# Kernel tuning notes

Measured on AMD Instinct MI355X. Metric: run time of the kernel, lower is better.

Reference implementation:

```python
import jax, jax.numpy as jnp
from jax import lax
import numpy as np

B, C, H, W = 32, 3, 224, 224
NUM_CLASSES = 100
K = 3  # kernel size
OUT1 = 32


def _bn(x, g, b, m, v, eps=1e-5):
    # eval-mode batchnorm over channel dim of NCHW
    inv = g / jnp.sqrt(v + eps)
    return x * inv[None, :, None, None] + (b - m * inv)[None, :, None, None]


def _conv(x, w, pad=1):
    return lax.conv_general_dilated(
        x, w, (1, 1), ((pad, pad), (pad, pad)),
        dimension_numbers=('NCHW', 'OIHW', 'NCHW'))


def _maxpool2(x):
    return lax.reduce_window(x, -jnp.inf, lax.max, (1, 1, 2, 2), (1, 1, 2, 2), 'VALID')


def setup_inputs() -> dict:
    key = jax.random.key(0)
    ks = jax.random.split(key, 32)
    n = lambda k, s, sc=0.05: jax.random.normal(k, s, jnp.float32) * sc
    u = lambda k, s: jax.random.uniform(k, s, jnp.float32, 0.5, 1.5)
    inp = {
        'x': jax.random.normal(ks[0], (B, C, H, W), jnp.float32),
        # weight_gen MLP: Linear(3,128)->ReLU->Linear(128,256)->ReLU->Linear(256, 32*3*3*3)
        'w1': n(ks[1], (128, C)), 'b1': n(ks[2], (128,)),
        'w2': n(ks[3], (256, 128)), 'b2': n(ks[4], (256,)),
        'w3': n(ks[5], (OUT1 * C * K * K, 256)), 'b3': n(ks[6], (OUT1 * C * K * K,)),
        # bias_gen: Linear(3, 32)
        'wb': n(ks[7], (OUT1, C)), 'bb': n(ks[8], (OUT1,)),
        'conv2_w': n(ks[9], (64, 32, 3, 3)), 'conv2_b': n(ks[10], (64,)),
        'conv3_w': n(ks[11], (128, 64, 3, 3)), 'conv3_b': n(ks[12], (128,)),
        'bn1_g': 1.0 + n(ks[13], (32,)), 'bn1_b': n(ks[14], (32,)), 'bn1_m': n(ks[15], (32,)), 'bn1_v': u(ks[16], (32,)),
        'bn2_g': 1.0 + n(ks[17], (64,)), 'bn2_b': n(ks[18], (64,)), 'bn2_m': n(ks[19], (64,)), 'bn2_v': u(ks[20], (64,)),
        'bn3_g': 1.0 + n(ks[21], (128,)), 'bn3_b': n(ks[22], (128,)), 'bn3_m': n(ks[23], (128,)), 'bn3_v': u(ks[24], (128,)),
        'fc_w': n(ks[25], (NUM_CLASSES, 128)), 'fc_b': n(ks[26], (NUM_CLASSES,)),
    }
    return inp


def reference(x, w1, b1, w2, b2, w3, b3, wb, bb, conv2_w, conv2_b, conv3_w, conv3_b,
              bn1_g, bn1_b, bn1_m, bn1_v, bn2_g, bn2_b, bn2_m, bn2_v,
              bn3_g, bn3_b, bn3_m, bn3_v, fc_w, fc_b):
    Bx = x.shape[0]
    # DynamicConv2D: channel indicator is all-ones since C == max_in_channels
    ind = jnp.ones((Bx, C), x.dtype)
    h = jax.nn.relu(ind @ w1.T + b1)
    h = jax.nn.relu(h @ w2.T + b2)
    dyn_w = (h @ w3.T + b3).reshape(Bx, OUT1, C, K, K)  # per-sample [O,I,k,k]
    dyn_b = ind @ wb.T + bb                             # per-sample [O]
    # vmap over batch: one single-image conv per sample with its own weights
    y = jax.vmap(lambda xi, wi, bi: _conv(xi[None], wi)[0] + bi[:, None, None])(x, dyn_w, dyn_b)
    y = jax.nn.relu(_bn(y, bn1_g, bn1_b, bn1_m, bn1_v))
    y = _maxpool2(y)
    y = jax.nn.relu(_bn(_conv(y, conv2_w) + conv2_b[None, :, None, None], bn2_g, bn2_b, bn2_m, bn2_v))
    y = _maxpool2(y)
    y = jax.nn.relu(_bn(_conv(y, conv3_w) + conv3_b[None, :, None, None], bn3_g, bn3_b, bn3_m, bn3_v))
    y = y.mean(axis=(2, 3))  # AdaptiveAvgPool2d((1,1)) + flatten
    # dropout is identity in eval
    return y @ fc_w.T + fc_b
```

## Files before the change

### kernel.cpp

```cpp
#include <hip/hip_runtime.h>
#include <hip/hip_bf16.h>

#define BATCH 32
#define HW1 224

typedef __attribute__((ext_vector_type(8))) short short8;
typedef __attribute__((ext_vector_type(4))) float floatx4;

static __device__ __forceinline__ unsigned short f2bf(float f) {
    unsigned int u = __float_as_uint(f);
    unsigned int r = (u + 0x7fffu + ((u >> 16) & 1u)) >> 16;
    return (unsigned short)r;
}

__global__ __launch_bounds__(256) void gen_dynw_repack(
    const float* __restrict__ w1, const float* __restrict__ b1,
    const float* __restrict__ w2, const float* __restrict__ b2,
    const float* __restrict__ w3, const float* __restrict__ b3,
    const float* __restrict__ conv2_w, const float* __restrict__ conv3_w,
    const float* __restrict__ wb, const float* __restrict__ bb,
    const float* __restrict__ conv2_b, const float* __restrict__ conv3_b,
    const float* __restrict__ bn1_g, const float* __restrict__ bn1_b,
    const float* __restrict__ bn1_m, const float* __restrict__ bn1_v,
    const float* __restrict__ bn2_g, const float* __restrict__ bn2_b,
    const float* __restrict__ bn2_m, const float* __restrict__ bn2_v,
    const float* __restrict__ bn3_g, const float* __restrict__ bn3_b,
    const float* __restrict__ bn3_m, const float* __restrict__ bn3_v,
    float* __restrict__ dwt,
    unsigned short* __restrict__ wrep2, unsigned short* __restrict__ wrep3,
    float* __restrict__ bn1_s, float* __restrict__ bn1_t,
    float* __restrict__ bn2_s, float* __restrict__ bn2_t,
    float* __restrict__ bn3_s, float* __restrict__ bn3_t,
    float* __restrict__ feat)
{
    __shared__ float h1s[128];
    __shared__ float h2s[256];
    const int blk = blockIdx.x;
    const int t = threadIdx.x;
    if (blk < 216) {
        if (t < 128) {
            float s = b1[t] + w1[t*3+0] + w1[t*3+1] + w1[t*3+2];
            h1s[t] = fmaxf(s, 0.f);
        }
        __syncthreads();
        {
            float s = b2[t];
            const float* wr = w2 + (size_t)t*128;
#pragma unroll 4
            for (int k = 0; k < 128; k += 4) {
                float4 wv = *(const float4*)(wr + k);
                s = fmaf(wv.x, h1s[k  ], s);
                s = fmaf(wv.y, h1s[k+1], s);
                s = fmaf(wv.z, h1s[k+2], s);
                s = fmaf(wv.w, h1s[k+3], s);
            }
            h2s[t] = fmaxf(s, 0.f);
        }
        __syncthreads();
        const int wave = t >> 6, lane = t & 63;
        const int row = blk*4 + wave;
        float4 wv = *(const float4*)(w3 + (size_t)row*256 + lane*4);
        float4 hv = *(const float4*)&h2s[lane*4];
        float s = wv.x*hv.x + wv.y*hv.y + wv.z*hv.z + wv.w*hv.w;
#pragma unroll
        for (int m = 1; m < 64; m <<= 1) s += __shfl_xor(s, m);
        if (lane == 0) {
            int oc = row / 27, tap = row - oc*27;
            dwt[tap*32 + oc] = s + b3[row];
        }
    } else if (blk < 576) {
        const int i = (blk - 216)*256 + t;
        const int N2 = 9*64*32;
        if (i < N2) {
            int tp = i / (64*32); int rem = i - tp*(64*32);
            int oc = rem >> 5, ic = rem & 31;
            wrep2[i] = f2bf(conv2_w[(oc*32 + ic)*9 + tp]);
        } else {
            int j = i - N2;
            int tp = j / (128*64); int rem = j - tp*(128*64);
            int oc = rem >> 6, ic = rem & 63;
            wrep3[j] = f2bf(conv3_w[(oc*64 + ic)*9 + tp]);
        }
    } else {
        if (t < 32) {
            float dynb = bb[t] + wb[t*3+0] + wb[t*3+1] + wb[t*3+2];
            float s = bn1_g[t] / sqrtf(bn1_v[t] + 1e-5f);
            bn1_s[t] = s;
            bn1_t[t] = (dynb - bn1_m[t]) * s + bn1_b[t];
        }
        if (t < 64) {
            float s = bn2_g[t] / sqrtf(bn2_v[t] + 1e-5f);
            bn2_s[t] = s;
            bn2_t[t] = (conv2_b[t] - bn2_m[t]) * s + bn2_b[t];
        }
        if (t < 128) {
            float s = bn3_g[t] / sqrtf(bn3_v[t] + 1e-5f);
            bn3_s[t] = s;
            bn3_t[t] = (conv3_b[t] - bn3_m[t]) * s + bn3_b[t];
        }
        for (int i = t; i < BATCH*128; i += 256) feat[i] = 0.f;
    }
}

__global__ __launch_bounds__(256) void conv1_pool(
    const float* __restrict__ x, const float* __restrict__ dwt,
    const float* __restrict__ bn_s, const float* __restrict__ bn_t,
    unsigned short* __restrict__ act1)
{
    __shared__ __align__(16) unsigned short sp[18*18*4];
    __shared__ __align__(16) unsigned short swA[32*32];
    __shared__ __align__(16) unsigned short swB[32*32];

    const int tid = threadIdx.x;
    const int bx = blockIdx.x, by = blockIdx.y, b = blockIdx.z;
    const int gx0 = bx*16 - 1, gy0 = by*16 - 1;
    const float* xb = x + (size_t)b * 3 * HW1 * HW1;

    for (int i = tid; i < 1024; i += 256) { swA[i] = 0; swB[i] = 0; }

    for (int i = tid; i < 324; i += 256) {
        int r = i / 18, c = i - r*18;
        int gy = gy0 + r, gx = gx0 + c;
        unsigned short v0 = 0, v1 = 0, v2 = 0;
        if ((unsigned)gy < HW1 && (unsigned)gx < HW1) {
            const float* pp = xb + gy*HW1 + gx;
            v0 = f2bf(pp[0]);
            v1 = f2bf(pp[HW1*HW1]);
            v2 = f2bf(pp[2*HW1*HW1]);
        }
        unsigned int lo = (unsigned int)v0 | ((unsigned int)v1 << 16);
        unsigned int hi = (unsigned int)v2;
        *(uint2*)&sp[i*4] = make_uint2(lo, hi);
    }
    __syncthreads();

    for (int i = tid; i < 864; i += 256) {
        int tap = i >> 5, oc = i & 31;
        int ic = tap / 9, kk = tap - ic*9;
        int ky = kk / 3, kx = kk - ky*3;
        unsigned short v = f2bf(dwt[i]);
        if (kk == 8)      swB[oc*32 + ic] = v;
        else if (kx < 2)  swA[oc*32 + ky*8 + kx*4 + ic] = v;
        else              swA[oc*32 + 3*8  + ky*4 + ic] = v;
    }
    __syncthreads();

    const int lane = tid & 63, wave = tid >> 6;
    const int n = lane & 15, quad = lane >> 4;

    short8 afrA[2], afrB[2];
#pragma unroll
    for (int h = 0; h < 2; ++h) {
        afrA[h] = *(const short8*)&swA[((h*16 + n)*32) + quad*8];
        afrB[h] = *(const short8*)&swB[((h*16 + n)*32) + quad*8];
    }
    float4 sv[2], tv[2];
#pragma unroll
    for (int h = 0; h < 2; ++h) {
        sv[h] = *(const float4*)(bn_s + h*16 + quad*4);
        tv[h] = *(const float4*)(bn_t + h*16 + quad*4);
    }

    union U { short8 s8; uint2 u2[2]; };

    const int y0w = wave*4;
    float ev[2][4];

#pragma unroll
    for (int yi = 0; yi < 4; ++yi) {
        const int y = y0w + yi;
        int r0 = (quad < 3) ? (y + quad) : y;
        int c0 = (quad < 3) ? n : (n + 2);
        int r1 = (quad < 3) ? (y + quad) : (y + 1);
        int c1 = (quad < 3) ? (n + 1) : (n + 2);
        U bf1;
        bf1.u2[0] = *(const uint2*)&sp[(r0*18 + c0)*4];
        bf1.u2[1] = *(const uint2*)&sp[(r1*18 + c1)*4];
        U bf2;
        bf2.u2[0] = *(const uint2*)&sp[((y+2)*18 + (n+2))*4];
        bf2.u2[1] = bf2.u2[0];

        float vr[2][4];
#pragma unroll
        for (int h = 0; h < 2; ++h) {
            floatx4 acc = {0.f, 0.f, 0.f, 0.f};
            acc = __builtin_amdgcn_mfma_f32_16x16x32_bf16(afrA[h], bf1.s8, acc, 0, 0, 0);
            acc = __builtin_amdgcn_mfma_f32_16x16x32_bf16(afrB[h], bf2.s8, acc, 0, 0, 0);
            float sj[4] = {sv[h].x, sv[h].y, sv[h].z, sv[h].w};
            float tj[4] = {tv[h].x, tv[h].y, tv[h].z, tv[h].w};
#pragma unroll
            for (int j = 0; j < 4; ++j)
                vr[h][j] = fmaxf(fmaf(acc[j], sj[j], tj[j]), 0.f);
        }

        if ((yi & 1) == 0) {
#pragma unroll
            for (int h = 0; h < 2; ++h)
#pragma unroll
                for (int j = 0; j < 4; ++j) ev[h][j] = vr[h][j];
        } else {
            int py = by*8 + ((y0w + yi) >> 1);
            int px = bx*8 + (n >> 1);
            unsigned short* dstp =
                act1 + ((size_t)((b*112 + py)*112 + px))*32 + quad*4;
#pragma unroll
            for (int h = 0; h < 2; ++h) {
                unsigned int pk[2];
#pragma unroll
                for (int j = 0; j < 4; ++j) {
                    float m = fmaxf(vr[h][j], ev[h][j]);
                    m = fmaxf(m, __shfl_xor(m, 1));
                    unsigned short us = f2bf(m);
                    if (j & 1) pk[j >> 1] |= ((unsigned int)us) << 16;
                    else       pk[j >> 1]  = us;
                }
                if (!(n & 1)) *(uint2*)(dstp + h*16) = *(uint2*)pk;
            }
        }
    }
}

__global__ __launch_bounds__(256) void conv2_mfma(
    const unsigned short* __restrict__ act1,
    const unsigned short* __restrict__ wrep,
    const float* __restrict__ bn_s, const float* __restrict__ bn_t,
    unsigned short* __restrict__ act2)
{
    constexpr int IC = 32, OC = 64, H = 112;
    __shared__ __align__(16) short lds[4*18*18*8];

    const int tid = threadIdx.x;
    const int b = blockIdx.z;
    const int cx0 = blockIdx.x*16, cy0 = blockIdx.y*16;
    const unsigned short* ab = act1 + (size_t)b*H*H*IC;

    for (int s = tid; s < 4*324; s += 256) {
        int ck = s / 324; int rem = s - ck*324;
        int y = rem / 18, xx = rem - y*18;
        int gy = cy0 - 1 + y, gx = cx0 - 1 + xx;
        uint4 v = {0,0,0,0};
        if ((unsigned)gy < H && (unsigned)gx < H)
            v = *(const uint4*)(ab + (size_t)(gy*H + gx)*IC + ck*8);
        *(uint4*)&lds[s*8] = v;
    }

    const int lane = tid & 63, wave = tid >> 6;
    const int n = lane & 15, quad = lane >> 4;
    const int oc0w = wave * 16;

    short8 afr[9];
#pragma unroll
    for (int t = 0; t < 9; ++t)
        afr[t] = *(const short8*)(wrep + (size_t)(t*OC + oc0w + n)*IC + quad*8);

    float4 sv = *(const float4*)(bn_s + oc0w + quad*4);
    float4 tv = *(const float4*)(bn_t + oc0w + quad*4);
    float sj[4] = {sv.x, sv.y, sv.z, sv.w};
    float tj[4] = {tv.x, tv.y, tv.z, tv.w};

    __syncthreads();

    floatx4 acc[3];
    float ev[4];

#pragma unroll
    for (int r = 0; r < 18; ++r) {
        const short* rp = &lds[((quad*18 + r)*18 + n)*8];
        short8 w0 = *(const short8*)(rp);
        short8 w1 = *(const short8*)(rp + 8);
        short8 w2 = *(const short8*)(rp + 16);

        if (r < 16) {
            floatx4 a = {0.f,0.f,0.f,0.f};
            a = __builtin_amdgcn_mfma_f32_16x16x32_bf16(afr[0], w0, a, 0, 0, 0);
            a = __builtin_amdgcn_mfma_f32_16x16x32_bf16(afr[1], w1, a, 0, 0, 0);
            a = __builtin_amdgcn_mfma_f32_16x16x32_bf16(afr[2], w2, a, 0, 0, 0);
            acc[r % 3] = a;
        }
        if (r >= 1 && r <= 16) {
            int y = r - 1;
            floatx4 a = acc[y % 3];
            a = __builtin_amdgcn_mfma_f32_16x16x32_bf16(afr[3], w0, a, 0, 0, 0);
            a = __builtin_amdgcn_mfma_f32_16x16x32_bf16(afr[4], w1, a, 0, 0, 0);
            a = __builtin_amdgcn_mfma_f32_16x16x32_bf16(afr[5], w2, a, 0, 0, 0);
            acc[y % 3] = a;
        }
        if (r >= 2) {
            int y = r - 2;
            floatx4 a = acc[y % 3];
            a = __builtin_amdgcn_mfma_f32_16x16x32_bf16(afr[6], w0, a, 0, 0, 0);
            a = __builtin_amdgcn_mfma_f32_16x16x32_bf16(afr[7], w1, a, 0, 0, 0);
            a = __builtin_amdgcn_mfma_f32_16x16x32_bf16(afr[8], w2, a, 0, 0, 0);

            float v[4];
#pragma unroll
            for (int j = 0; j < 4; ++j)
                v[j] = fmaxf(fmaf(a[j], sj[j], tj[j]), 0.f);

            if ((y & 1) == 0) {
#pragma unroll
                for (int j = 0; j < 4; ++j) ev[j] = v[j];
            } else {
                unsigned int pk[2];
#pragma unroll
                for (int j = 0; j < 4; ++j) {
                    float m = fmaxf(v[j], ev[j]);
                    m = fmaxf(m, __shfl_xor(m, 1));
                    unsigned short us = f2bf(m);
                    if (j & 1) pk[j >> 1] |= ((unsigned int)us) << 16;
                    else       pk[j >> 1]  = us;
                }
                if (!(n & 1)) {
                    int py = (cy0 >> 1) + (y >> 1), px = (cx0 >> 1) + (n >> 1);
                    unsigned short* dstp =
                        act2 + ((size_t)((b*56 + py)*56 + px))*OC + oc0w + quad*4;
                    *(uint2*)dstp = *(uint2*)pk;
                }
            }
        }
    }
}

__global__ __launch_bounds__(256) void conv3_mfma(
    const unsigned short* __restrict__ act2,
    const unsigned short* __restrict__ wrep,
    const float* __restrict__ bn_s, const float* __restrict__ bn_t,
    float* __restrict__ feat)
{
    constexpr int IC = 64, OC = 128, H = 56;
    __shared__ __align__(16) short lds[8*16*18*8];

    const int tid = threadIdx.x;
    const int b = blockIdx.z >> 1, half = blockIdx.z & 1;
    const int cx0 = blockIdx.x*16, cy0 = blockIdx.y*14;
    const unsigned short* ab = act2 + (size_t)b*H*H*IC;

    for (int s = tid; s < 8*16*18; s += 256) {
        int ck = s / (16*18); int rem = s - ck*(16*18);
        int y = rem / 18, xx = rem - y*18;
        int gy = cy0 - 1 + y, gx = cx0 - 1 + xx;
        uint4 v = {0,0,0,0};
        if ((unsigned)gy < H && (unsigned)gx < H)
            v = *(const uint4*)(ab + (size_t)(gy*H + gx)*IC + ck*8);
        *(uint4*)&lds[s*8] = v;
    }

    const int lane = tid & 63, wave = tid >> 6;
    const int n = lane & 15, quad = lane >> 4;
    const int oc0w = half*64 + wave*16;

    short8 afr[18];
#pragma unroll
    for (int t = 0; t < 9; ++t)
#pragma unroll
        for (int kc = 0; kc < 2; ++kc)
            afr[t*2 + kc] = *(const short8*)(wrep + (size_t)(t*OC + oc0w + n)*IC + kc*32 + quad*8);

    float4 sv = *(const float4*)(bn_s + oc0w + quad*4);
    float4 tv = *(const float4*)(bn_t + oc0w + quad*4);
    float sj[4] = {sv.x, sv.y, sv.z, sv.w};
    float tj[4] = {tv.x, tv.y, tv.z, tv.w};

    __syncthreads();

    float sum[4] = {0.f, 0.f, 0.f, 0.f};
    const bool vx = (cx0 + n) < H;
    floatx4 acc[3];

#pragma unroll
    for (int r = 0; r < 16; ++r) {
        const short* p0 = &lds[((quad*16     + r)*18 + n)*8];
        const short* p1 = &lds[(((4+quad)*16 + r)*18 + n)*8];
        short8 a0 = *(const short8*)(p0);
        short8 a1 = *(const short8*)(p0 + 8);
        short8 a2 = *(const short8*)(p0 + 16);
        short8 b0 = *(const short8*)(p1);
        short8 b1 = *(const short8*)(p1 + 8);
        short8 b2 = *(const short8*)(p1 + 16);

        if (r < 14) {
            floatx4 a = {0.f,0.f,0.f,0.f};
            a = __builtin_amdgcn_mfma_f32_16x16x32_bf16(afr[0], a0, a, 0, 0, 0);
            a = __builtin_amdgcn_mfma_f32_16x16x32_bf16(afr[1], b0, a, 0, 0, 0);
            a = __builtin_amdgcn_mfma_f32_16x16x32_bf16(afr[2], a1, a, 0, 0, 0);
            a = __builtin_amdgcn_mfma_f32_16x16x32_bf16(afr[3], b1, a, 0, 0, 0);
            a = __builtin_amdgcn_mfma_f32_16x16x32_bf16(afr[4], a2, a, 0, 0, 0);
            a = __builtin_amdgcn_mfma_f32_16x16x32_bf16(afr[5], b2, a, 0, 0, 0);
            acc[r % 3] = a;
        }
        if (r >= 1 && r <= 14) {
            int y = r - 1;
            floatx4 a = acc[y % 3];
            a = __builtin_amdgcn_mfma_f32_16x16x32_bf16(afr[6],  a0, a, 0, 0, 0);
            a = __builtin_amdgcn_mfma_f32_16x16x32_bf16(afr[7],  b0, a, 0, 0, 0);
            a = __builtin_amdgcn_mfma_f32_16x16x32_bf16(afr[8],  a1, a, 0, 0, 0);
            a = __builtin_amdgcn_mfma_f32_16x16x32_bf16(afr[9],  b1, a, 0, 0, 0);
            a = __builtin_amdgcn_mfma_f32_16x16x32_bf16(afr[10], a2, a, 0, 0, 0);
            a = __builtin_amdgcn_mfma_f32_16x16x32_bf16(afr[11], b2, a, 0, 0, 0);
            acc[y % 3] = a;
        }
        if (r >= 2) {
            int y = r - 2;
            floatx4 a = acc[y % 3];
            a = __builtin_amdgcn_mfma_f32_16x16x32_bf16(afr[12], a0, a, 0, 0, 0);
            a = __builtin_amdgcn_mfma_f32_16x16x32_bf16(afr[13], b0, a, 0, 0, 0);
            a = __builtin_amdgcn_mfma_f32_16x16x32_bf16(afr[14], a1, a, 0, 0, 0);
            a = __builtin_amdgcn_mfma_f32_16x16x32_bf16(afr[15], b1, a, 0, 0, 0);
            a = __builtin_amdgcn_mfma_f32_16x16x32_bf16(afr[16], a2, a, 0, 0, 0);
            a = __builtin_amdgcn_mfma_f32_16x16x32_bf16(afr[17], b2, a, 0, 0, 0);
            if (vx) {
#pragma unroll
                for (int j = 0; j < 4; ++j)
                    sum[j] += fmaxf(fmaf(a[j], sj[j], tj[j]), 0.f);
            }
        }
    }
#pragma unroll
    for (int j = 0; j < 4; ++j) {
        sum[j] += __shfl_xor(sum[j], 1);
        sum[j] += __shfl_xor(sum[j], 2);
        sum[j] += __shfl_xor(sum[j], 4);
        sum[j] += __shfl_xor(sum[j], 8);
    }
    if (n == 0) {
#pragma unroll
        for (int j = 0; j < 4; ++j)
            atomicAdd(&feat[b*128 + oc0w + quad*4 + j], sum[j]);
    }
}

__global__ __launch_bounds__(256) void fc_kernel(
    const float* __restrict__ feat, const float* __restrict__ fc_w,
    const float* __restrict__ fc_b, float* __restrict__ out)
{
    int i = blockIdx.x * 256 + threadIdx.x;
    if (i >= BATCH*100) return;
    int b = i / 100, n = i - b*100;
    const float* f = feat + b*128;
    const float* w = fc_w + n*128;
    float s = 0.f;
#pragma unroll 4
    for (int k = 0; k < 128; ++k) s = fmaf(f[k], w[k], s);
    out[i] = s * (1.f/3136.f) + fc_b[n];
}

extern "C" void kernel_launch(void* const* d_in, const int* in_sizes, int n_in,
                              void* d_out, int out_size, void* d_ws, size_t ws_size,
                              hipStream_t stream)
{
    const float* x       = (const float*)d_in[0];
    const float* w1      = (const float*)d_in[1];
    const float* b1      = (const float*)d_in[2];
    const float* w2      = (const float*)d_in[3];
    const float* b2      = (const float*)d_in[4];
    const float* w3      = (const float*)d_in[5];
    const float* b3      = (const float*)d_in[6];
    const float* wb      = (const float*)d_in[7];
    const float* bb      = (const float*)d_in[8];
    const float* conv2_w = (const float*)d_in[9];
    const float* conv2_b = (const float*)d_in[10];
    const float* conv3_w = (const float*)d_in[11];
    const float* conv3_b = (const float*)d_in[12];
    const float* bn1_g = (const float*)d_in[13];
    const float* bn1_b = (const float*)d_in[14];
    const float* bn1_m = (const float*)d_in[15];
    const float* bn1_v = (const float*)d_in[16];
    const float* bn2_g = (const float*)d_in[17];
    const float* bn2_b = (const float*)d_in[18];
    const float* bn2_m = (const float*)d_in[19];
    const float* bn2_v = (const float*)d_in[20];
    const float* bn3_g = (const float*)d_in[21];
    const float* bn3_b = (const float*)d_in[22];
    const float* bn3_m = (const float*)d_in[23];
    const float* bn3_v = (const float*)d_in[24];
    const float* fc_w  = (const float*)d_in[25];
    const float* fc_b  = (const float*)d_in[26];
    float* out = (float*)d_out;

    char* wsb = (char*)d_ws;
    float* ws    = (float*)d_ws;
    float* dwt   = ws;
    float* bn1_s = ws + 864;
    float* bn1_t = ws + 896;
    float* bn2_s = ws + 928;
    float* bn2_t = ws + 992;
    float* bn3_s = ws + 1056;
    float* bn3_t = ws + 1184;
    float* feat  = ws + 1312;
    unsigned short* wrep2 = (unsigned short*)(wsb + 32768);
    unsigned short* wrep3 = (unsigned short*)(wsb + 69632);
    unsigned short* act1  = (unsigned short*)(wsb + 262144);
    unsigned short* act2  = (unsigned short*)(wsb + 262144 + 25690112);

    gen_dynw_repack<<<577, 256, 0, stream>>>(
        w1, b1, w2, b2, w3, b3, conv2_w, conv3_w,
        wb, bb, conv2_b, conv3_b,
        bn1_g, bn1_b, bn1_m, bn1_v, bn2_g, bn2_b, bn2_m, bn2_v,
        bn3_g, bn3_b, bn3_m, bn3_v,
        dwt, wrep2, wrep3,
        bn1_s, bn1_t, bn2_s, bn2_t, bn3_s, bn3_t, feat);

    conv1_pool<<<dim3(14, 14, BATCH), 256, 0, stream>>>(
        x, dwt, bn1_s, bn1_t, act1);

    conv2_mfma<<<dim3(7, 7, BATCH), 256, 0, stream>>>(
        act1, wrep2, bn2_s, bn2_t, act2);

    conv3_mfma<<<dim3(4, 4, BATCH*2), 256, 0, stream>>>(
        act2, wrep3, bn3_s, bn3_t, feat);

    fc_kernel<<<(BATCH*100 + 255)/256, 256, 0, stream>>>(feat, fc_w, fc_b, out);
}
```

Measured before the change: 190.4 us.

## Prepack dynamic conv1 weights as bf16 MFMA panels and widen conv1 tiles

The dynamic-weight generator now writes conv1 weights straight into bf16 MFMA A-fragment panels in global memory, computed by a single block. conv1_pool therefore no longer zero-fills or repacks weights into shared memory per block and loads its fragments directly. conv1 tiles are also widened to 32 columns, so each block handles two 16-wide column halves and the grid is halved in x. In exchange, the w3 matvec runs serially in one block (2048 entries, each a 256-long dot product per thread), which may lengthen the prologue kernel's critical path.

```diff
diff --git a/kernel.cpp b/kernel.cpp
--- a/kernel.cpp
+++ b/kernel.cpp
@@ -13,7 +13,7 @@
     return (unsigned short)r;
 }
 
-__global__ __launch_bounds__(256) void gen_dynw_repack(
+__global__ __launch_bounds__(256) void gen_repack(
     const float* __restrict__ w1, const float* __restrict__ b1,
     const float* __restrict__ w2, const float* __restrict__ b2,
     const float* __restrict__ w3, const float* __restrict__ b3,
@@ -26,7 +26,7 @@
     const float* __restrict__ bn2_m, const float* __restrict__ bn2_v,
     const float* __restrict__ bn3_g, const float* __restrict__ bn3_b,
     const float* __restrict__ bn3_m, const float* __restrict__ bn3_v,
-    float* __restrict__ dwt,
+    unsigned short* __restrict__ wpan,
     unsigned short* __restrict__ wrep2, unsigned short* __restrict__ wrep3,
     float* __restrict__ bn1_s, float* __restrict__ bn1_t,
     float* __restrict__ bn2_s, float* __restrict__ bn2_t,
@@ -37,7 +37,38 @@
     __shared__ float h2s[256];
     const int blk = blockIdx.x;
     const int t = threadIdx.x;
-    if (blk < 216) {
+    if (blk < 360) {
+        const int i = blk*256 + t;
+        const int N2 = 9*64*32;
+        if (i < N2) {
+            int tp = i / (64*32); int rem = i - tp*(64*32);
+            int oc = rem >> 5, ic = rem & 31;
+            wrep2[i] = f2bf(conv2_w[(oc*32 + ic)*9 + tp]);
+        } else {
+            int j = i - N2;
+            int tp = j / (128*64); int rem = j - tp*(128*64);
+            int oc = rem >> 6, ic = rem & 63;
+            wrep3[j] = f2bf(conv3_w[(oc*64 + ic)*9 + tp]);
+        }
+    } else if (blk == 360) {
+        if (t < 32) {
+            float dynb = bb[t] + wb[t*3+0] + wb[t*3+1] + wb[t*3+2];
+            float s = bn1_g[t] / sqrtf(bn1_v[t] + 1e-5f);
+            bn1_s[t] = s;
+            bn1_t[t] = (dynb - bn1_m[t]) * s + bn1_b[t];
+        }
+        if (t < 64) {
+            float s = bn2_g[t] / sqrtf(bn2_v[t] + 1e-5f);
+            bn2_s[t] = s;
+            bn2_t[t] = (conv2_b[t] - bn2_m[t]) * s + bn2_b[t];
+        }
+        if (t < 128) {
+            float s = bn3_g[t] / sqrtf(bn3_v[t] + 1e-5f);
+            bn3_s[t] = s;
+            bn3_t[t] = (conv3_b[t] - bn3_m[t]) * s + bn3_b[t];
+        }
+        for (int i = t; i < BATCH*128; i += 256) feat[i] = 0.f;
+    } else {
         if (t < 128) {
             float s = b1[t] + w1[t*3+0] + w1[t*3+1] + w1[t*3+2];
             h1s[t] = fmaxf(s, 0.f);
@@ -57,69 +88,56 @@
             h2s[t] = fmaxf(s, 0.f);
         }
         __syncthreads();
-        const int wave = t >> 6, lane = t & 63;
-        const int row = blk*4 + wave;
-        float4 wv = *(const float4*)(w3 + (size_t)row*256 + lane*4);
-        float4 hv = *(const float4*)&h2s[lane*4];
-        float s = wv.x*hv.x + wv.y*hv.y + wv.z*hv.z + wv.w*hv.w;
-#pragma unroll
-        for (int m = 1; m < 64; m <<= 1) s += __shfl_xor(s, m);
-        if (lane == 0) {
-            int oc = row / 27, tap = row - oc*27;
-            dwt[tap*32 + oc] = s + b3[row];
-        }
-    } else if (blk < 576) {
-        const int i = (blk - 216)*256 + t;
-        const int N2 = 9*64*32;
-        if (i < N2) {
-            int tp = i / (64*32); int rem = i - tp*(64*32);
-            int oc = rem >> 5, ic = rem & 31;
-            wrep2[i] = f2bf(conv2_w[(oc*32 + ic)*9 + tp]);
-        } else {
-            int j = i - N2;
-            int tp = j / (128*64); int rem = j - tp*(128*64);
-            int oc = rem >> 6, ic = rem & 63;
-            wrep3[j] = f2bf(conv3_w[(oc*64 + ic)*9 + tp]);
-        }
-    } else {
-        if (t < 32) {
-            float dynb = bb[t] + wb[t*3+0] + wb[t*3+1] + wb[t*3+2];
-            float s = bn1_g[t] / sqrtf(bn1_v[t] + 1e-5f);
-            bn1_s[t] = s;
-            bn1_t[t] = (dynb - bn1_m[t]) * s + bn1_b[t];
-        }
-        if (t < 64) {
-            float s = bn2_g[t] / sqrtf(bn2_v[t] + 1e-5f);
-            bn2_s[t] = s;
-            bn2_t[t] = (conv2_b[t] - bn2_m[t]) * s + bn2_b[t];
-        }
-        if (t < 128) {
-            float s = bn3_g[t] / sqrtf(bn3_v[t] + 1e-5f);
-            bn3_s[t] = s;
-            bn3_t[t] = (conv3_b[t] - bn3_m[t]) * s + bn3_b[t];
-        }
-        for (int i = t; i < BATCH*128; i += 256) feat[i] = 0.f;
+        for (int i = t; i < 2048; i += 256) {
+            int panel = i >> 10, rem = i & 1023;
+            int oc = rem >> 5, k = rem & 31;
+            int tap = -1;
+            if (panel == 0) {
+                int quad = k >> 3, s = k & 7;
+                if (quad < 3) {
+                    int kx = s >> 2, ic = s & 3;
+                    if (ic < 3) tap = ic*9 + quad*3 + kx;
+                } else {
+                    int ky = s >> 2, ic = s & 3;
+                    if (ic < 3) tap = ic*9 + ky*3 + 2;
+                }
+            } else {
+                if (k < 3) tap = k*9 + 8;
+            }
+            unsigned short v = 0;
+            if (tap >= 0) {
+                int row = oc*27 + tap;
+                const float* wr = w3 + (size_t)row*256;
+                float s = b3[row];
+#pragma unroll 4
+                for (int kk = 0; kk < 256; kk += 4) {
+                    float4 wv = *(const float4*)(wr + kk);
+                    s = fmaf(wv.x, h2s[kk  ], s);
+                    s = fmaf(wv.y, h2s[kk+1], s);
+                    s = fmaf(wv.z, h2s[kk+2], s);
+                    s = fmaf(wv.w, h2s[kk+3], s);
+                }
+                v = f2bf(s);
+            }
+            wpan[i] = v;
+        }
     }
 }
 
 __global__ __launch_bounds__(256) void conv1_pool(
-    const float* __restrict__ x, const float* __restrict__ dwt,
+    const float* __restrict__ x, const unsigned short* __restrict__ wpan,
     const float* __restrict__ bn_s, const float* __restrict__ bn_t,
     unsigned short* __restrict__ act1)
 {
-    __shared__ __align__(16) unsigned short sp[18*18*4];
-    __shared__ __align__(16) unsigned short swA[32*32];
-    __shared__ __align__(16) unsigned short swB[32*32];
+    __shared__ __align__(16) unsigned short sp[18*34*4];
 
     const int tid = threadIdx.x;
     const int bx = blockIdx.x, by = blockIdx.y, b = blockIdx.z;
-    const int gx0 = bx*16 - 1, gy0 = by*16 - 1;
+    const int gx0 = bx*32 - 1, gy0 = by*16 - 1;
     const float* xb = x + (size_t)b * 3 * HW1 * HW1;
 
-    for (int i = tid; i < 1024; i += 256) { swA[i] = 0; swB[i] = 0; }
-
-    for (int i = tid; i < 324; i += 256) {
-        int r = i / 18, c = i - r*18;
+    for (int i = tid; i < 18*34; i += 256) {
+        int r = i / 34, c = i - r*34;
         int gy = gy0 + r, gx = gx0 + c;
         unsigned short v0 = 0, v1 = 0, v2 = 0;
         if ((unsigned)gy < HW1 && (unsigned)gx < HW1) {
@@ -132,18 +150,6 @@
         unsigned int hi = (unsigned int)v2;
         *(uint2*)&sp[i*4] = make_uint2(lo, hi);
     }
-    __syncthreads();
-
-    for (int i = tid; i < 864; i += 256) {
-        int tap = i >> 5, oc = i & 31;
-        int ic = tap / 9, kk = tap - ic*9;
-        int ky = kk / 3, kx = kk - ky*3;
-        unsigned short v = f2bf(dwt[i]);
-        if (kk == 8)      swB[oc*32 + ic] = v;
-        else if (kx < 2)  swA[oc*32 + ky*8 + kx*4 + ic] = v;
-        else              swA[oc*32 + 3*8  + ky*4 + ic] = v;
-    }
-    __syncthreads();
 
     const int lane = tid & 63, wave = tid >> 6;
     const int n = lane & 15, quad = lane >> 4;
@@ -151,8 +157,8 @@
     short8 afrA[2], afrB[2];
 #pragma unroll
     for (int h = 0; h < 2; ++h) {
-        afrA[h] = *(const short8*)&swA[((h*16 + n)*32) + quad*8];
-        afrB[h] = *(const short8*)&swB[((h*16 + n)*32) + quad*8];
+        afrA[h] = *(const short8*)&wpan[((h*16 + n)*32) + quad*8];
+        afrB[h] = *(const short8*)&wpan[1024 + ((h*16 + n)*32) + quad*8];
     }
     float4 sv[2], tv[2];
 #pragma unroll
@@ -161,60 +167,70 @@
         tv[h] = *(const float4*)(bn_t + h*16 + quad*4);
     }
 
+    __syncthreads();
+
     union U { short8 s8; uint2 u2[2]; };
 
     const int y0w = wave*4;
-    float ev[2][4];
+    float ev[2][2][4];
 
 #pragma unroll
     for (int yi = 0; yi < 4; ++yi) {
         const int y = y0w + yi;
-        int r0 = (quad < 3) ? (y + quad) : y;
-        int c0 = (quad < 3) ? n : (n + 2);
-        int r1 = (quad < 3) ? (y + quad) : (y + 1);
-        int c1 = (quad < 3) ? (n + 1) : (n + 2);
-        U bf1;
-        bf1.u2[0] = *(const uint2*)&sp[(r0*18 + c0)*4];
-        bf1.u2[1] = *(const uint2*)&sp[(r1*18 + c1)*4];
-        U bf2;
-        bf2.u2[0] = *(const uint2*)&sp[((y+2)*18 + (n+2))*4];
-        bf2.u2[1] = bf2.u2[0];
-
-        float vr[2][4];
-#pragma unroll
-        for (int h = 0; h < 2; ++h) {
-            floatx4 acc = {0.f, 0.f, 0.f, 0.f};
-            acc = __builtin_amdgcn_mfma_f32_16x16x32_bf16(afrA[h], bf1.s8, acc, 0, 0, 0);
-            acc = __builtin_amdgcn_mfma_f32_16x16x32_bf16(afrB[h], bf2.s8, acc, 0, 0, 0);
-            float sj[4] = {sv[h].x, sv[h].y, sv[h].z, sv[h].w};
-            float tj[4] = {tv[h].x, tv[h].y, tv[h].z, tv[h].w};
-#pragma unroll
-            for (int j = 0; j < 4; ++j)
-                vr[h][j] = fmaxf(fmaf(acc[j], sj[j], tj[j]), 0.f);
+        float vr[2][2][4];
+#pragma unroll
+        for (int hx = 0; hx < 2; ++hx) {
+            const int cb = n + hx*16;
+            int r0 = (quad < 3) ? (y + quad) : y;
+            int c0 = (quad < 3) ? cb : (cb + 2);
+            int r1 = (quad < 3) ? (y + quad) : (y + 1);
+            int c1 = (quad < 3) ? (cb + 1) : (cb + 2);
+            U bf1;
+            bf1.u2[0] = *(const uint2*)&sp[(r0*34 + c0)*4];
+            bf1.u2[1] = *(const uint2*)&sp[(r1*34 + c1)*4];
+            U bf2;
+            bf2.u2[0] = *(const uint2*)&sp[((y+2)*34 + (cb+2))*4];
+            bf2.u2[1] = bf2.u2[0];
+#pragma unroll
+            for (int h = 0; h < 2; ++h) {
+                floatx4 acc = {0.f, 0.f, 0.f, 0.f};
+                acc = __builtin_amdgcn_mfma_f32_16x16x32_bf16(afrA[h], bf1.s8, acc, 0, 0, 0);
+                acc = __builtin_amdgcn_mfma_f32_16x16x32_bf16(afrB[h], bf2.s8, acc, 0, 0, 0);
+                float sj[4] = {sv[h].x, sv[h].y, sv[h].z, sv[h].w};
+                float tj[4] = {tv[h].x, tv[h].y, tv[h].z, tv[h].w};
+#pragma unroll
+                for (int j = 0; j < 4; ++j)
+                    vr[hx][h][j] = fmaxf(fmaf(acc[j], sj[j], tj[j]), 0.f);
+            }
         }
 
         if ((yi & 1) == 0) {
 #pragma unroll
-            for (int h = 0; h < 2; ++h)
-#pragma unroll
-                for (int j = 0; j < 4; ++j) ev[h][j] = vr[h][j];
+            for (int hx = 0; hx < 2; ++hx)
+#pragma unroll
+                for (int h = 0; h < 2; ++h)
+#pragma unroll
+                    for (int j = 0; j < 4; ++j) ev[hx][h][j] = vr[hx][h][j];
         } else {
             int py = by*8 + ((y0w + yi) >> 1);
-            int px = bx*8 + (n >> 1);
-            unsigned short* dstp =
-                act1 + ((size_t)((b*112 + py)*112 + px))*32 + quad*4;
-#pragma unroll
-            for (int h = 0; h < 2; ++h) {
-                unsigned int pk[2];
-#pragma unroll
-                for (int j = 0; j < 4; ++j) {
-                    float m = fmaxf(vr[h][j], ev[h][j]);
-                    m = fmaxf(m, __shfl_xor(m, 1));
-                    unsigned short us = f2bf(m);
-                    if (j & 1) pk[j >> 1] |= ((unsigned int)us) << 16;
-                    else       pk[j >> 1]  = us;
+#pragma unroll
+            for (int hx = 0; hx < 2; ++hx) {
+                int px = bx*16 + hx*8 + (n >> 1);
+                unsigned short* dstp =
+                    act1 + ((size_t)((b*112 + py)*112 + px))*32 + quad*4;
+#pragma unroll
+                for (int h = 0; h < 2; ++h) {
+                    unsigned int pk[2];
+#pragma unroll
+                    for (int j = 0; j < 4; ++j) {
+                        float m = fmaxf(vr[hx][h][j], ev[hx][h][j]);
+                        m = fmaxf(m, __shfl_xor(m, 1));
+                        unsigned short us = f2bf(m);
+                        if (j & 1) pk[j >> 1] |= ((unsigned int)us) << 16;
+                        else       pk[j >> 1]  = us;
+                    }
+                    if (!(n & 1)) *(uint2*)(dstp + h*16) = *(uint2*)pk;
                 }
-                if (!(n & 1)) *(uint2*)(dstp + h*16) = *(uint2*)pk;
             }
         }
     }
@@ -479,7 +495,6 @@
 
     char* wsb = (char*)d_ws;
     float* ws    = (float*)d_ws;
-    float* dwt   = ws;
     float* bn1_s = ws + 864;
     float* bn1_t = ws + 896;
     float* bn2_s = ws + 928;
@@ -487,21 +502,22 @@
     float* bn3_s = ws + 1056;
     float* bn3_t = ws + 1184;
     float* feat  = ws + 1312;
+    unsigned short* wpan  = (unsigned short*)(wsb + 24576);
     unsigned short* wrep2 = (unsigned short*)(wsb + 32768);
     unsigned short* wrep3 = (unsigned short*)(wsb + 69632);
     unsigned short* act1  = (unsigned short*)(wsb + 262144);
     unsigned short* act2  = (unsigned short*)(wsb + 262144 + 25690112);
 
-    gen_dynw_repack<<<577, 256, 0, stream>>>(
+    gen_repack<<<362, 256, 0, stream>>>(
         w1, b1, w2, b2, w3, b3, conv2_w, conv3_w,
         wb, bb, conv2_b, conv3_b,
         bn1_g, bn1_b, bn1_m, bn1_v, bn2_g, bn2_b, bn2_m, bn2_v,
         bn3_g, bn3_b, bn3_m, bn3_v,
-        dwt, wrep2, wrep3,
+        wpan, wrep2, wrep3,
         bn1_s, bn1_t, bn2_s, bn2_t, bn3_s, bn3_t, feat);
 
-    conv1_pool<<<dim3(14, 14, BATCH), 256, 0, stream>>>(
-        x, dwt, bn1_s, bn1_t, act1);
+    conv1_pool<<<dim3(7, 14, BATCH), 256, 0, stream>>>(
+        x, wpan, bn1_s, bn1_t, act1);
 
     conv2_mfma<<<dim3(7, 7, BATCH), 256, 0, stream>>>(
         act1, wrep2, bn2_s, bn2_t, act2);
```

Result: slower. 226.3 us (+18.8%).
